# Optimization experiments

Hardware: AMD Instinct MI355X
Metric: run time of the kernel (lower is better)

Reference implementation:

```python
import jax, jax.numpy as jnp
import numpy as np

B, S, D, H, F = 4, 1024, 2048, 16, 8192
HD = D // H  # head dim = 128
EPS = 1e-5


def layer_norm(x, w, b):
    mu = jnp.mean(x, axis=-1, keepdims=True)
    var = jnp.mean(jnp.square(x - mu), axis=-1, keepdims=True)
    return (x - mu) * jax.lax.rsqrt(var + EPS) * w + b


def setup_inputs() -> dict:
    key = jax.random.key(0)
    ks = jax.random.split(key, 12)
    s = 0.02  # realistic init scale for weights
    return {
        "x": jax.random.normal(ks[0], (B, S, D), jnp.float32),
        "attention_mask": jnp.zeros((B, 1, 1, S), jnp.float32),
        "wq": jax.random.normal(ks[1], (D, D), jnp.float32) * s,
        "bq": jax.random.normal(ks[2], (D,), jnp.float32) * s,
        "wk": jax.random.normal(ks[3], (D, D), jnp.float32) * s,
        "bk": jax.random.normal(ks[4], (D,), jnp.float32) * s,
        "wv": jax.random.normal(ks[5], (D, D), jnp.float32) * s,
        "bv": jax.random.normal(ks[6], (D,), jnp.float32) * s,
        "wo": jax.random.normal(ks[7], (D, D), jnp.float32) * s,
        "bo": jax.random.normal(ks[8], (D,), jnp.float32) * s,
        "ln1_w": jnp.ones((D,), jnp.float32),
        "ln1_b": jnp.zeros((D,), jnp.float32),
        "wi": jax.random.normal(ks[9], (F, D), jnp.float32) * s,
        "bi": jax.random.normal(ks[10], (F,), jnp.float32) * s,
        "wo2": jax.random.normal(ks[11], (D, F), jnp.float32) * s,
        "bo2": jnp.zeros((D,), jnp.float32),
        "ln2_w": jnp.ones((D,), jnp.float32),
        "ln2_b": jnp.zeros((D,), jnp.float32),
    }


def reference(x, attention_mask, wq, bq, wk, bk, wv, bv, wo, bo,
              ln1_w, ln1_b, wi, bi, wo2, bo2, ln2_w, ln2_b):
    # --- self attention ---
    q = (jnp.einsum('bsd,ed->bse', x, wq) + bq).reshape(B, S, H, HD).transpose(0, 2, 1, 3)
    k = (jnp.einsum('bsd,ed->bse', x, wk) + bk).reshape(B, S, H, HD).transpose(0, 2, 1, 3)
    v = (jnp.einsum('bsd,ed->bse', x, wv) + bv).reshape(B, S, H, HD).transpose(0, 2, 1, 3)
    scores = jnp.einsum('bhqd,bhkd->bhqk', q, k) / jnp.sqrt(jnp.float32(HD))
    scores = scores + attention_mask  # additive mask, broadcast over heads/query
    probs = jax.nn.softmax(scores, axis=-1)
    ctx = jnp.einsum('bhqk,bhkd->bhqd', probs, v)
    ctx = ctx.transpose(0, 2, 1, 3).reshape(B, S, D)
    # --- attention output: dense + bias + residual + LayerNorm ---
    attn_out = layer_norm(jnp.einsum('bsd,ed->bse', ctx, wo) + bo + x, ln1_w, ln1_b)
    # --- FFN: intermediate dense + bias, GELU, output dense + bias + residual + LN ---
    inter = jnp.einsum('bsd,fd->bsf', attn_out, wi) + bi
    h = jax.nn.gelu(inter, approximate=False)
    out = layer_norm(jnp.einsum('bsf,df->bsd', h, wo2) + bo2 + attn_out, ln2_w, ln2_b)
    return out
```

## Files before the change

kernel.cpp:

```cpp
#include <hip/hip_runtime.h>
#include <hip/hip_bf16.h>
#include <cstdint>
#include <cstddef>

typedef __attribute__((ext_vector_type(8))) short short8;
typedef __attribute__((ext_vector_type(4))) float f32x4;

#define DEV static __device__ __forceinline__

constexpr int kS = 1024, kD = 2048, kH = 16, kHD = 128, kF = 8192;
constexpr int kM = 4096;
constexpr float kEPS = 1e-5f;

constexpr size_t SZ_DD   = (size_t)kD * kD * 2;
constexpr size_t SZ_FD   = (size_t)kF * kD * 2;
constexpr size_t SZ_MD16 = (size_t)kM * kD * 2;
constexpr size_t SZ_MD32 = (size_t)kM * kD * 4;
constexpr size_t OFF_WQ  = 0;
constexpr size_t OFF_WK  = OFF_WQ + SZ_DD;
constexpr size_t OFF_WV  = OFF_WK + SZ_DD;
constexpr size_t OFF_WO  = OFF_WV + SZ_DD;
constexpr size_t OFF_WI  = OFF_WO + SZ_DD;
constexpr size_t OFF_WO2 = OFF_WI + SZ_FD;
constexpr size_t OFF_XB  = OFF_WO2 + SZ_FD;
constexpr size_t OFF_Q   = OFF_XB + SZ_MD16;
constexpr size_t OFF_K   = OFF_Q + SZ_MD16;
constexpr size_t OFF_V   = OFF_K + SZ_MD16;
constexpr size_t OFF_H   = OFF_XB;
constexpr size_t OFF_CTX = OFF_V + SZ_MD16;
constexpr size_t OFF_Y1  = OFF_CTX + SZ_MD16;
constexpr size_t OFF_A1B = OFF_Y1 + SZ_MD32;
constexpr size_t OFF_Y2  = OFF_A1B + SZ_MD16;
constexpr size_t WS_NEED = OFF_Y2 + SZ_MD32;

DEV void gload16(const void* g, void* l) {
  __builtin_amdgcn_global_load_lds(
      (const __attribute__((address_space(1))) unsigned int*)g,
      (__attribute__((address_space(3))) unsigned int*)l, 16, 0, 0);
}

__global__ void cvt_bf16(const float* __restrict__ in, __hip_bfloat16* __restrict__ out, int n4) {
  int stride = gridDim.x * blockDim.x;
  for (int i = blockIdx.x * blockDim.x + threadIdx.x; i < n4; i += stride) {
    float4 v = reinterpret_cast<const float4*>(in)[i];
    union { ushort4 u; __hip_bfloat16 h[4]; } o;
    o.h[0] = __float2bfloat16(v.x);
    o.h[1] = __float2bfloat16(v.y);
    o.h[2] = __float2bfloat16(v.z);
    o.h[3] = __float2bfloat16(v.w);
    reinterpret_cast<ushort4*>(out)[i] = o.u;
  }
}

template <int MODE>
__global__ __launch_bounds__(512, 2)
void gemm256(const __hip_bfloat16* __restrict__ A,
             const __hip_bfloat16* __restrict__ Bt,
             const float* __restrict__ bias,
             float* __restrict__ out0, float* __restrict__ out1,
             void* __restrict__ outb,
             int M, int N, int K, int kLen) {
  __shared__ __align__(16) char lds[131072];
  const int tid = threadIdx.x;
  const int lane = tid & 63, w = tid >> 6;
  const int wm = w >> 2, wn = w & 3;
  const int hw = w >> 2;
  const int lg = lane >> 4, lr = lane & 15;
  const int gy = M >> 8, gx = N >> 8;
  const int nwg = gridDim.x, orig = blockIdx.x;
  const int l = (orig & 7) * (nwg >> 3) + (orig >> 3);
  const int tilesPer = gx * gy;
  const int spl = l / tilesPer;
  const int rem = l - spl * tilesPer;
  const int bx = rem / gy, by = rem - bx * gy;
  const int m0 = by * 256, n0 = bx * 256;
  const int k0 = spl * kLen;
  const int NT = kLen >> 6;

  const char* gs[8];
  #pragma unroll
  for (int h = 0; h < 4; ++h) {
    const __hip_bfloat16* src = (h < 2) ? A : Bt;
    const int r0 = ((h < 2) ? m0 : n0) + (h & 1) * 128;
    #pragma unroll
    for (int i = 0; i < 2; ++i) {
      int c = i * 512 + tid;
      int row = c >> 3, slot = c & 7;
      gs[h * 2 + i] =
          (const char*)(src + (size_t)(r0 + row) * K + k0 + (slot ^ (row & 7)) * 8);
    }
  }

#define STAGE(P, H, TOFF)                                                          \
  {                                                                                \
    char* dstb = lds + (((H) < 2) ? 0 : 65536) + (P) * 32768 + ((H) & 1) * 16384;  \
    gload16(gs[(H) * 2 + 0] + (TOFF) * 128, dstb + (0 * 512 + tid) * 16);          \
    gload16(gs[(H) * 2 + 1] + (TOFF) * 128, dstb + (1 * 512 + tid) * 16);          \
  }

  auto ldA = [&](int P, int qm, int mr, int kk) {
    int row = qm * 128 + wm * 64 + mr * 16 + lr;
    return *reinterpret_cast<const short8*>(
        lds + P * 32768 + row * 128 + (((kk * 4 + lg) ^ (row & 7)) * 16));
  };
  auto ldB = [&](int P, int qn, int nr, int kk) {
    int row = qn * 128 + wn * 32 + nr * 16 + lr;
    return *reinterpret_cast<const short8*>(
        lds + 65536 + P * 32768 + row * 128 + (((kk * 4 + lg) ^ (row & 7)) * 16));
  };

  f32x4 acc[4][4][2] = {};

#define MFMA_HALF(p, kk, B)                                                     \
  _Pragma("unroll")                                                             \
  for (int mi = 0; mi < 4; ++mi)                                                \
    _Pragma("unroll")                                                           \
    for (int ni = 0; ni < 2; ++ni)                                              \
      acc[p][mi][ni] = __builtin_amdgcn_mfma_f32_16x16x32_bf16(                 \
          av[kk][mi], B[kk][ni], acc[p][mi][ni], 0, 0, 0);

#define WAIT_LGKM(n)                                                            \
  asm volatile("s_waitcnt lgkmcnt(" #n ")" ::: "memory");                       \
  __builtin_amdgcn_sched_barrier(0);

#define TILE_BODY(P, PF)                                                        \
  {                                                                             \
          \
    asm volatile("s_waitcnt vmcnt(0)" ::: "memory");                            \
    __builtin_amdgcn_s_barrier();                                               \
                          \
    _Pragma("unroll")                                                           \
    for (int i = 0; i < 4; ++i) av[0][i] = ldA(P, hw, i, 0);                    \
    _Pragma("unroll")                                                           \
    for (int i = 0; i < 2; ++i) b0[0][i] = ldB(P, hw, i, 0);                    \
    _Pragma("unroll")                                                           \
    for (int i = 0; i < 4; ++i) av[1][i] = ldA(P, hw, i, 1);                    \
    _Pragma("unroll")                                                           \
    for (int i = 0; i < 2; ++i) b0[1][i] = ldB(P, hw, i, 1);                    \
    if (PF) { STAGE((P) ^ 1, 0, 1 + (P)) STAGE((P) ^ 1, 2, 1 + (P)) }           \
    WAIT_LGKM(6)                                                                \
    __builtin_amdgcn_s_setprio(1);                                              \
    MFMA_HALF(0, 0, b0)                                                         \
    WAIT_LGKM(0)                                                                \
    MFMA_HALF(0, 1, b0)                                                         \
    __builtin_amdgcn_s_setprio(0);                                              \
                        \
    _Pragma("unroll")                                                           \
    for (int i = 0; i < 2; ++i) b1[0][i] = ldB(P, 1 - hw, i, 0);                \
    _Pragma("unroll")                                                           \
    for (int i = 0; i < 2; ++i) b1[1][i] = ldB(P, 1 - hw, i, 1);                \
    if (PF) { STAGE((P) ^ 1, 3, 1 + (P)) STAGE((P) ^ 1, 1, 1 + (P)) }           \
    WAIT_LGKM(2)                                                                \
    __builtin_amdgcn_s_setprio(1);                                              \
    MFMA_HALF(1, 0, b1)                                                         \
    WAIT_LGKM(0)                                                                \
    MFMA_HALF(1, 1, b1)                                                         \
    __builtin_amdgcn_s_setprio(0);                                              \
                                           \
    _Pragma("unroll")                                                           \
    for (int i = 0; i < 4; ++i) av[0][i] = ldA(P, 1 - hw, i, 0);                \
    _Pragma("unroll")                                                           \
    for (int i = 0; i < 4; ++i) av[1][i] = ldA(P, 1 - hw, i, 1);                \
    WAIT_LGKM(4)                                                                \
    __builtin_amdgcn_s_setprio(1);                                              \
    MFMA_HALF(2, 0, b1)                                                         \
    WAIT_LGKM(0)                                                                \
    MFMA_HALF(2, 1, b1)                                                         \
    __builtin_amdgcn_s_setprio(0);                                              \
                                          \
    _Pragma("unroll")                                                           \
    for (int i = 0; i < 2; ++i) b0[0][i] = ldB(P, hw, i, 0);                    \
    _Pragma("unroll")                                                           \
    for (int i = 0; i < 2; ++i) b0[1][i] = ldB(P, hw, i, 1);                    \
    WAIT_LGKM(2)                                                                \
    __builtin_amdgcn_s_setprio(1);                                              \
    MFMA_HALF(3, 0, b0)                                                         \
    WAIT_LGKM(0)                                                                \
    MFMA_HALF(3, 1, b0)                                                         \
    __builtin_amdgcn_s_setprio(0);                                              \
  }

  STAGE(0, 0, 0) STAGE(0, 2, 0) STAGE(0, 3, 0) STAGE(0, 1, 0)

  for (int t2 = 0; t2 < NT; t2 += 2) {
    short8 av[2][4], b0[2][2], b1[2][2];
    TILE_BODY(0, true)
    TILE_BODY(1, (t2 + 2 < NT))
    #pragma unroll
    for (int j = 0; j < 8; ++j) gs[j] += 256;
  }
#undef TILE_BODY
#undef MFMA_HALF
#undef WAIT_LGKM
#undef STAGE

  #pragma unroll
  for (int p = 0; p < 4; ++p) {
    const int qm = (p < 2) ? hw : 1 - hw;
    const int qn = (p == 0 || p == 3) ? hw : 1 - hw;
    #pragma unroll
    for (int ni = 0; ni < 2; ++ni) {
      int col = n0 + qn * 128 + wn * 32 + ni * 16 + lr;
      float bvv = 0.f;
      if constexpr (MODE != 3) bvv = bias[col];
      #pragma unroll
      for (int mi = 0; mi < 4; ++mi) {
        int row0 = m0 + qm * 128 + wm * 64 + mi * 16 + lg * 4;
        #pragma unroll
        for (int r = 0; r < 4; ++r) {
          int row = row0 + r;
          float val = acc[p][mi][ni][r] + bvv;
          if constexpr (MODE == 0) {
            int which = col >> 11;
            int d = col & 2047;
            int hh = d >> 7, hd = d & 127;
            int bb = row >> 10, ss = row & 1023;
            __hip_bfloat16* base = (__hip_bfloat16*)outb + (size_t)which * ((size_t)kM * kD);
            base[(((size_t)(bb * kH + hh)) * kS + ss) * kHD + hd] = __float2bfloat16(val);
          } else if constexpr (MODE == 2) {
            float g = 0.5f * val * (1.0f + erff(val * 0.70710678118654752f));
            ((__hip_bfloat16*)outb)[(size_t)row * N + col] = __float2bfloat16(g);
          } else {
            float* o = spl ? out1 : out0;
            o[(size_t)row * N + col] = val;
          }
        }
      }
    }
  }
}

__global__ __launch_bounds__(512, 4)
void attn_fwd(const __hip_bfloat16* __restrict__ q,
              const __hip_bfloat16* __restrict__ k,
              const __hip_bfloat16* __restrict__ v,
              const float* __restrict__ mask,
              __hip_bfloat16* __restrict__ ctx) {
  __shared__ __align__(16) char Ks[2][64 * 256];
  __shared__ __align__(16) char Vt[2][128 * 128];
  __shared__ __align__(16) char Ps[8][2048];
  const int tid = threadIdx.x, lane = tid & 63, w = tid >> 6;
  const int lg = lane >> 4, lr = lane & 15;
  const int orig = blockIdx.x;
  const int l = (orig & 7) * 64 + (orig >> 3);
  const int qt = l & 7, bh = l >> 3;
  const int b = bh >> 4;
  const int s4 = tid >> 5, hd4 = tid & 31;

  short8 qf[4];
  {
    const __hip_bfloat16* qp =
        q + ((size_t)bh * kS + qt * 128 + w * 16 + lr) * kHD + lg * 8;
    #pragma unroll
    for (int kk = 0; kk < 4; ++kk) qf[kk] = *reinterpret_cast<const short8*>(qp + kk * 32);
  }

  auto stageK = [&](int bufi, int t) {
    #pragma unroll
    for (int i = 0; i < 2; ++i) {
      int c = i * 512 + tid;
      int row = c >> 4, slot = c & 15;
      gload16(k + ((size_t)bh * kS + t * 64 + row) * kHD + (slot ^ (row & 15)) * 8,
              Ks[bufi] + c * 16);
    }
  };
  union VU { uint2 u; ushort s[4]; };
  VU vr[4];
  auto loadV = [&](int t) {
    #pragma unroll
    for (int i = 0; i < 4; ++i)
      vr[i].u = *reinterpret_cast<const uint2*>(
          v + ((size_t)bh * kS + t * 64 + s4 * 4 + i) * kHD + hd4 * 4);
  };
  auto writeV = [&](int bufi) {
    #pragma unroll
    for (int j = 0; j < 4; ++j) {
      int hd = hd4 * 4 + j;
      ushort4 o;
      o.x = vr[0].s[j]; o.y = vr[1].s[j]; o.z = vr[2].s[j]; o.w = vr[3].s[j];
      *reinterpret_cast<ushort4*>(
          Vt[bufi] + hd * 128 + (((s4 >> 1) ^ (hd & 7)) << 4) + ((s4 & 1) << 3)) = o;
    }
  };

  f32x4 o[8] = {};
  float mrun[4], lrun[4];
  #pragma unroll
  for (int r = 0; r < 4; ++r) { mrun[r] = -1e30f; lrun[r] = 0.f; }
  const float scale = 0.08838834764831845f;

  stageK(0, 0);
  loadV(0);
  writeV(0);
  __syncthreads();

  int buf = 0;
  for (int t = 0; t < 16; ++t) {
    if (t + 1 < 16) { stageK(buf ^ 1, t + 1); loadV(t + 1); }

    f32x4 sacc[4] = {};
    #pragma unroll
    for (int j = 0; j < 4; ++j) {
      int key = j * 16 + lr;
      #pragma unroll
      for (int kk = 0; kk < 4; ++kk) {
        short8 bfrag = *reinterpret_cast<const short8*>(
            Ks[buf] + key * 256 + (((kk * 4 + lg) ^ (key & 15)) * 16));
        sacc[j] = __builtin_amdgcn_mfma_f32_16x16x32_bf16(qf[kk], bfrag, sacc[j], 0, 0, 0);
      }
    }
    float sarr[4][4];
    #pragma unroll
    for (int j = 0; j < 4; ++j) {
      float mv = mask[(size_t)b * kS + t * 64 + j * 16 + lr];
      #pragma unroll
      for (int r = 0; r < 4; ++r) sarr[j][r] = sacc[j][r] * scale + mv;
    }
    #pragma unroll
    for (int r = 0; r < 4; ++r) {
      float tm = fmaxf(fmaxf(sarr[0][r], sarr[1][r]), fmaxf(sarr[2][r], sarr[3][r]));
      #pragma unroll
      for (int d = 1; d < 16; d <<= 1) tm = fmaxf(tm, __shfl_xor(tm, d));
      float mnew = fmaxf(mrun[r], tm);
      float alpha = __expf(mrun[r] - mnew);
      mrun[r] = mnew;
      float rs = 0.f;
      #pragma unroll
      for (int j = 0; j < 4; ++j) {
        float p = __expf(sarr[j][r] - mnew);
        sarr[j][r] = p;
        rs += p;
      }
      #pragma unroll
      for (int d = 1; d < 16; d <<= 1) rs += __shfl_xor(rs, d);
      lrun[r] = lrun[r] * alpha + rs;
      #pragma unroll
      for (int n = 0; n < 8; ++n) o[n][r] *= alpha;
    }
    #pragma unroll
    for (int r = 0; r < 4; ++r) {
      int qr = lg * 4 + r;
      #pragma unroll
      for (int j = 0; j < 4; ++j)
        *reinterpret_cast<__hip_bfloat16*>(
            Ps[w] + ((qr * 128 + (j * 16 + lr) * 2) ^ ((qr & 7) << 4))) =
            __float2bfloat16(sarr[j][r]);
    }
    #pragma unroll
    for (int kk2 = 0; kk2 < 2; ++kk2) {
      short8 pa = *reinterpret_cast<const short8*>(
          Ps[w] + ((lr * 128 + kk2 * 64 + lg * 16) ^ ((lr & 7) << 4)));
      #pragma unroll
      for (int n = 0; n < 8; ++n) {
        int hd = n * 16 + lr;
        short8 vb = *reinterpret_cast<const short8*>(
            Vt[buf] + hd * 128 + (((kk2 * 4 + lg) ^ (hd & 7)) * 16));
        o[n] = __builtin_amdgcn_mfma_f32_16x16x32_bf16(pa, vb, o[n], 0, 0, 0);
      }
    }
    if (t + 1 < 16) writeV(buf ^ 1);
    __syncthreads();
    buf ^= 1;
  }

  const int h = bh & 15;
  #pragma unroll
  for (int r = 0; r < 4; ++r) {
    float inv = 1.0f / lrun[r];
    int srow = qt * 128 + w * 16 + lg * 4 + r;
    __hip_bfloat16* cp = ctx + ((size_t)b * kS + srow) * kD + h * 128 + lr;
    #pragma unroll
    for (int n = 0; n < 8; ++n) cp[n * 16] = __float2bfloat16(o[n][r] * inv);
  }
}

template <bool WB16>
__global__ void ln_fuse(const float* __restrict__ p0, const float* __restrict__ p1,
                        const float* __restrict__ bias, const float* __restrict__ res,
                        const float* __restrict__ w, const float* __restrict__ b,
                        float* __restrict__ outf, __hip_bfloat16* __restrict__ outb) {
  const int row = blockIdx.x, tid = threadIdx.x;
  const size_t base = (size_t)row * kD;
  float v[8];
  #pragma unroll
  for (int i = 0; i < 2; ++i) {
    int c4 = tid * 2 + i;
    float4 a  = reinterpret_cast<const float4*>(p0 + base)[c4];
    float4 bb = reinterpret_cast<const float4*>(p1 + base)[c4];
    float4 rr = reinterpret_cast<const float4*>(res + base)[c4];
    float4 bs = reinterpret_cast<const float4*>(bias)[c4];
    v[i * 4 + 0] = a.x + bb.x + rr.x + bs.x;
    v[i * 4 + 1] = a.y + bb.y + rr.y + bs.y;
    v[i * 4 + 2] = a.z + bb.z + rr.z + bs.z;
    v[i * 4 + 3] = a.w + bb.w + rr.w + bs.w;
  }
  float s = 0.f;
  #pragma unroll
  for (int i = 0; i < 8; ++i) s += v[i];
  #pragma unroll
  for (int off = 32; off > 0; off >>= 1) s += __shfl_down(s, off);
  __shared__ float r1[4], r2[4];
  if ((tid & 63) == 0) r1[tid >> 6] = s;
  __syncthreads();
  float mean = (r1[0] + r1[1] + r1[2] + r1[3]) * (1.0f / kD);
  float qv = 0.f;
  #pragma unroll
  for (int i = 0; i < 8; ++i) { float d = v[i] - mean; qv += d * d; }
  #pragma unroll
  for (int off = 32; off > 0; off >>= 1) qv += __shfl_down(qv, off);
  if ((tid & 63) == 0) r2[tid >> 6] = qv;
  __syncthreads();
  float rstd = rsqrtf((r2[0] + r2[1] + r2[2] + r2[3]) * (1.0f / kD) + kEPS);
  #pragma unroll
  for (int i = 0; i < 8; ++i) {
    int col = tid * 8 + i;
    float ov = (v[i] - mean) * rstd * w[col] + b[col];
    outf[base + col] = ov;
    if constexpr (WB16) outb[base + col] = __float2bfloat16(ov);
  }
}

extern "C" void kernel_launch(void* const* d_in, const int* in_sizes, int n_in,
                              void* d_out, int out_size, void* d_ws, size_t ws_size,
                              hipStream_t stream) {
  (void)in_sizes; (void)n_in; (void)out_size;
  if (ws_size < WS_NEED) return;
  const float* x    = (const float*)d_in[0];
  const float* mask = (const float*)d_in[1];
  const float* wq   = (const float*)d_in[2];
  const float* bq   = (const float*)d_in[3];
  const float* wk   = (const float*)d_in[4];
  const float* bk   = (const float*)d_in[5];
  const float* wv   = (const float*)d_in[6];
  const float* bv   = (const float*)d_in[7];
  const float* wo   = (const float*)d_in[8];
  const float* bo   = (const float*)d_in[9];
  const float* l1w  = (const float*)d_in[10];
  const float* l1b  = (const float*)d_in[11];
  const float* wi   = (const float*)d_in[12];
  const float* bi   = (const float*)d_in[13];
  const float* wo2  = (const float*)d_in[14];
  const float* bo2  = (const float*)d_in[15];
  const float* l2w  = (const float*)d_in[16];
  const float* l2b  = (const float*)d_in[17];

  char* ws = (char*)d_ws;
  __hip_bfloat16* wqb  = (__hip_bfloat16*)(ws + OFF_WQ);
  __hip_bfloat16* wkb  = (__hip_bfloat16*)(ws + OFF_WK);
  __hip_bfloat16* wvb  = (__hip_bfloat16*)(ws + OFF_WV);
  __hip_bfloat16* wob  = (__hip_bfloat16*)(ws + OFF_WO);
  __hip_bfloat16* wib  = (__hip_bfloat16*)(ws + OFF_WI);
  __hip_bfloat16* wo2b = (__hip_bfloat16*)(ws + OFF_WO2);
  __hip_bfloat16* xb   = (__hip_bfloat16*)(ws + OFF_XB);
  __hip_bfloat16* qb   = (__hip_bfloat16*)(ws + OFF_Q);
  __hip_bfloat16* kb2  = (__hip_bfloat16*)(ws + OFF_K);
  __hip_bfloat16* vb2  = (__hip_bfloat16*)(ws + OFF_V);
  __hip_bfloat16* hb   = (__hip_bfloat16*)(ws + OFF_H);
  __hip_bfloat16* ctxb = (__hip_bfloat16*)(ws + OFF_CTX);
  __hip_bfloat16* a1b  = (__hip_bfloat16*)(ws + OFF_A1B);
  float* y1   = (float*)(ws + OFF_Y1);
  float* y2   = (float*)(ws + OFF_Y2);
  float* f2p  = (float*)(ws + OFF_WQ);
  float* bqkv = (float*)(ws + OFF_Y2);

  cvt_bf16<<<2048, 256, 0, stream>>>(x,   xb,   kM * kD / 4);
  cvt_bf16<<<1024, 256, 0, stream>>>(wq,  wqb,  kD * kD / 4);
  cvt_bf16<<<1024, 256, 0, stream>>>(wk,  wkb,  kD * kD / 4);
  cvt_bf16<<<1024, 256, 0, stream>>>(wv,  wvb,  kD * kD / 4);
  cvt_bf16<<<1024, 256, 0, stream>>>(wo,  wob,  kD * kD / 4);
  cvt_bf16<<<2048, 256, 0, stream>>>(wi,  wib,  kF * kD / 4);
  cvt_bf16<<<2048, 256, 0, stream>>>(wo2, wo2b, kF * kD / 4);
  hipMemcpyAsync(bqkv,          bq, kD * 4, hipMemcpyDeviceToDevice, stream);
  hipMemcpyAsync(bqkv + kD,     bk, kD * 4, hipMemcpyDeviceToDevice, stream);
  hipMemcpyAsync(bqkv + 2 * kD, bv, kD * 4, hipMemcpyDeviceToDevice, stream);

  dim3 blk(512);
  gemm256<0><<<dim3(384), blk, 0, stream>>>(
      xb, wqb, bqkv, nullptr, nullptr, qb, kM, 6144, kD, kD);
  attn_fwd<<<dim3(512), dim3(512), 0, stream>>>(qb, kb2, vb2, mask, ctxb);
  gemm256<3><<<dim3(256), blk, 0, stream>>>(
      ctxb, wob, nullptr, y1, y2, nullptr, kM, kD, kD, kD / 2);
  ln_fuse<true><<<kM, 256, 0, stream>>>(y1, y2, bo, x, l1w, l1b, y1, a1b);
  gemm256<2><<<dim3(512), blk, 0, stream>>>(
      a1b, wib, bi, nullptr, nullptr, hb, kM, kF, kD, kD);
  gemm256<3><<<dim3(256), blk, 0, stream>>>(
      hb, wo2b, nullptr, y2, f2p, nullptr, kM, kD, kF, kF / 2);
  ln_fuse<false><<<kM, 256, 0, stream>>>(y2, f2p, bo2, y1, l2w, l2b, (float*)d_out, nullptr);
}
```

Baseline: 672.5 us.

## Merge conversion kernels into one launch and double query rows per attention block

Replaces seven fp32-to-bf16 conversion launches plus three bias memcpys with a single cvt_all kernel that walks the contiguous workspace layout. The attention kernel now processes two 128-row query sub-tiles per block (256 blocks instead of 512), reusing each staged K/V tile for twice as many queries to halve K/V load and transpose work. The cost is doubled accumulator and softmax state per thread, which lowers occupancy (launch bounds drop from 4 to 2 blocks) and leaves fewer blocks to spread across CUs.

Measured after the change: 604.6 us. -10.1%, faster.

```diff
diff --git a/kernel.cpp b/kernel.cpp
--- a/kernel.cpp
+++ b/kernel.cpp
@@ -39,16 +39,37 @@
       (__attribute__((address_space(3))) unsigned int*)l, 16, 0, 0);
 }
 
-__global__ void cvt_bf16(const float* __restrict__ in, __hip_bfloat16* __restrict__ out, int n4) {
+__global__ void cvt_all(const float* __restrict__ x,  const float* __restrict__ wq,
+                        const float* __restrict__ wk, const float* __restrict__ wv,
+                        const float* __restrict__ wo, const float* __restrict__ wi,
+                        const float* __restrict__ wo2,
+                        const float* __restrict__ bq, const float* __restrict__ bk,
+                        const float* __restrict__ bv,
+                        __hip_bfloat16* __restrict__ outw, float* __restrict__ bqkv) {
+  constexpr int M1 = 1 << 20;
+  constexpr int NW = 14 * M1;
   int stride = gridDim.x * blockDim.x;
-  for (int i = blockIdx.x * blockDim.x + threadIdx.x; i < n4; i += stride) {
-    float4 v = reinterpret_cast<const float4*>(in)[i];
-    union { ushort4 u; __hip_bfloat16 h[4]; } o;
-    o.h[0] = __float2bfloat16(v.x);
-    o.h[1] = __float2bfloat16(v.y);
-    o.h[2] = __float2bfloat16(v.z);
-    o.h[3] = __float2bfloat16(v.w);
-    reinterpret_cast<ushort4*>(out)[i] = o.u;
+  for (int i = blockIdx.x * blockDim.x + threadIdx.x; i < NW + 1536; i += stride) {
+    if (i < NW) {
+      const float* src; int off;
+      if (i < 4 * M1)       { src = (i < M1) ? wq : (i < 2 * M1) ? wk : (i < 3 * M1) ? wv : wo;
+                              off = i & (M1 - 1); }
+      else if (i < 8 * M1)  { src = wi;  off = i - 4 * M1; }
+      else if (i < 12 * M1) { src = wo2; off = i - 8 * M1; }
+      else                  { src = x;   off = i - 12 * M1; }
+      float4 v = reinterpret_cast<const float4*>(src)[off];
+      union { ushort4 u; __hip_bfloat16 h[4]; } o;
+      o.h[0] = __float2bfloat16(v.x);
+      o.h[1] = __float2bfloat16(v.y);
+      o.h[2] = __float2bfloat16(v.z);
+      o.h[3] = __float2bfloat16(v.w);
+      reinterpret_cast<ushort4*>(outw)[i] = o.u;
+    } else {
+      int j = i - NW;
+      const float* src = (j < 512) ? bq : (j < 1024) ? bk : bv;
+      reinterpret_cast<float4*>(bqkv)[j] =
+          reinterpret_cast<const float4*>(src)[j & 511];
+    }
   }
 }
 
@@ -125,10 +146,8 @@
 
 #define TILE_BODY(P, PF)                                                        \
   {                                                                             \
-          \
     asm volatile("s_waitcnt vmcnt(0)" ::: "memory");                            \
     __builtin_amdgcn_s_barrier();                                               \
-                          \
     _Pragma("unroll")                                                           \
     for (int i = 0; i < 4; ++i) av[0][i] = ldA(P, hw, i, 0);                    \
     _Pragma("unroll")                                                           \
@@ -144,7 +163,6 @@
     WAIT_LGKM(0)                                                                \
     MFMA_HALF(0, 1, b0)                                                         \
     __builtin_amdgcn_s_setprio(0);                                              \
-                        \
     _Pragma("unroll")                                                           \
     for (int i = 0; i < 2; ++i) b1[0][i] = ldB(P, 1 - hw, i, 0);                \
     _Pragma("unroll")                                                           \
@@ -156,7 +174,6 @@
     WAIT_LGKM(0)                                                                \
     MFMA_HALF(1, 1, b1)                                                         \
     __builtin_amdgcn_s_setprio(0);                                              \
-                                           \
     _Pragma("unroll")                                                           \
     for (int i = 0; i < 4; ++i) av[0][i] = ldA(P, 1 - hw, i, 0);                \
     _Pragma("unroll")                                                           \
@@ -167,7 +184,6 @@
     WAIT_LGKM(0)                                                                \
     MFMA_HALF(2, 1, b1)                                                         \
     __builtin_amdgcn_s_setprio(0);                                              \
-                                          \
     _Pragma("unroll")                                                           \
     for (int i = 0; i < 2; ++i) b0[0][i] = ldB(P, hw, i, 0);                    \
     _Pragma("unroll")                                                           \
@@ -230,7 +246,7 @@
   }
 }
 
-__global__ __launch_bounds__(512, 4)
+__global__ __launch_bounds__(512, 2)
 void attn_fwd(const __hip_bfloat16* __restrict__ q,
               const __hip_bfloat16* __restrict__ k,
               const __hip_bfloat16* __restrict__ v,
@@ -242,17 +258,19 @@
   const int tid = threadIdx.x, lane = tid & 63, w = tid >> 6;
   const int lg = lane >> 4, lr = lane & 15;
   const int orig = blockIdx.x;
-  const int l = (orig & 7) * 64 + (orig >> 3);
-  const int qt = l & 7, bh = l >> 3;
+  const int l = (orig & 7) * 32 + (orig >> 3);
+  const int qp = l & 3, bh = l >> 2;
   const int b = bh >> 4;
   const int s4 = tid >> 5, hd4 = tid & 31;
 
-  short8 qf[4];
-  {
-    const __hip_bfloat16* qp =
-        q + ((size_t)bh * kS + qt * 128 + w * 16 + lr) * kHD + lg * 8;
-    #pragma unroll
-    for (int kk = 0; kk < 4; ++kk) qf[kk] = *reinterpret_cast<const short8*>(qp + kk * 32);
+  short8 qf[2][4];
+  #pragma unroll
+  for (int s = 0; s < 2; ++s) {
+    const __hip_bfloat16* qp_ =
+        q + ((size_t)bh * kS + qp * 256 + s * 128 + w * 16 + lr) * kHD + lg * 8;
+    #pragma unroll
+    for (int kk = 0; kk < 4; ++kk)
+      qf[s][kk] = *reinterpret_cast<const short8*>(qp_ + kk * 32);
   }
 
   auto stageK = [&](int bufi, int t) {
@@ -276,17 +294,19 @@
     #pragma unroll
     for (int j = 0; j < 4; ++j) {
       int hd = hd4 * 4 + j;
-      ushort4 o;
-      o.x = vr[0].s[j]; o.y = vr[1].s[j]; o.z = vr[2].s[j]; o.w = vr[3].s[j];
+      ushort4 o4;
+      o4.x = vr[0].s[j]; o4.y = vr[1].s[j]; o4.z = vr[2].s[j]; o4.w = vr[3].s[j];
       *reinterpret_cast<ushort4*>(
-          Vt[bufi] + hd * 128 + (((s4 >> 1) ^ (hd & 7)) << 4) + ((s4 & 1) << 3)) = o;
+          Vt[bufi] + hd * 128 + (((s4 >> 1) ^ (hd & 7)) << 4) + ((s4 & 1) << 3)) = o4;
     }
   };
 
-  f32x4 o[8] = {};
-  float mrun[4], lrun[4];
-  #pragma unroll
-  for (int r = 0; r < 4; ++r) { mrun[r] = -1e30f; lrun[r] = 0.f; }
+  f32x4 o[2][8] = {};
+  float mrun[2][4], lrun[2][4];
+  #pragma unroll
+  for (int s = 0; s < 2; ++s)
+    #pragma unroll
+    for (int r = 0; r < 4; ++r) { mrun[s][r] = -1e30f; lrun[s][r] = 0.f; }
   const float scale = 0.08838834764831845f;
 
   stageK(0, 0);
@@ -298,64 +318,69 @@
   for (int t = 0; t < 16; ++t) {
     if (t + 1 < 16) { stageK(buf ^ 1, t + 1); loadV(t + 1); }
 
-    f32x4 sacc[4] = {};
-    #pragma unroll
-    for (int j = 0; j < 4; ++j) {
-      int key = j * 16 + lr;
-      #pragma unroll
-      for (int kk = 0; kk < 4; ++kk) {
-        short8 bfrag = *reinterpret_cast<const short8*>(
-            Ks[buf] + key * 256 + (((kk * 4 + lg) ^ (key & 15)) * 16));
-        sacc[j] = __builtin_amdgcn_mfma_f32_16x16x32_bf16(qf[kk], bfrag, sacc[j], 0, 0, 0);
+    float mv[4];
+    #pragma unroll
+    for (int j = 0; j < 4; ++j) mv[j] = mask[(size_t)b * kS + t * 64 + j * 16 + lr];
+
+    #pragma unroll
+    for (int s = 0; s < 2; ++s) {
+      f32x4 sacc[4] = {};
+      #pragma unroll
+      for (int j = 0; j < 4; ++j) {
+        int key = j * 16 + lr;
+        #pragma unroll
+        for (int kk = 0; kk < 4; ++kk) {
+          short8 bfrag = *reinterpret_cast<const short8*>(
+              Ks[buf] + key * 256 + (((kk * 4 + lg) ^ (key & 15)) * 16));
+          sacc[j] = __builtin_amdgcn_mfma_f32_16x16x32_bf16(qf[s][kk], bfrag, sacc[j], 0, 0, 0);
+        }
       }
-    }
-    float sarr[4][4];
-    #pragma unroll
-    for (int j = 0; j < 4; ++j) {
-      float mv = mask[(size_t)b * kS + t * 64 + j * 16 + lr];
-      #pragma unroll
-      for (int r = 0; r < 4; ++r) sarr[j][r] = sacc[j][r] * scale + mv;
-    }
-    #pragma unroll
-    for (int r = 0; r < 4; ++r) {
-      float tm = fmaxf(fmaxf(sarr[0][r], sarr[1][r]), fmaxf(sarr[2][r], sarr[3][r]));
-      #pragma unroll
-      for (int d = 1; d < 16; d <<= 1) tm = fmaxf(tm, __shfl_xor(tm, d));
-      float mnew = fmaxf(mrun[r], tm);
-      float alpha = __expf(mrun[r] - mnew);
-      mrun[r] = mnew;
-      float rs = 0.f;
-      #pragma unroll
-      for (int j = 0; j < 4; ++j) {
-        float p = __expf(sarr[j][r] - mnew);
-        sarr[j][r] = p;
-        rs += p;
+      float sarr[4][4];
+      #pragma unroll
+      for (int j = 0; j < 4; ++j)
+        #pragma unroll
+        for (int r = 0; r < 4; ++r) sarr[j][r] = sacc[j][r] * scale + mv[j];
+      #pragma unroll
+      for (int r = 0; r < 4; ++r) {
+        float tm = fmaxf(fmaxf(sarr[0][r], sarr[1][r]), fmaxf(sarr[2][r], sarr[3][r]));
+        #pragma unroll
+        for (int d = 1; d < 16; d <<= 1) tm = fmaxf(tm, __shfl_xor(tm, d));
+        float mnew = fmaxf(mrun[s][r], tm);
+        float alpha = __expf(mrun[s][r] - mnew);
+        mrun[s][r] = mnew;
+        float rs = 0.f;
+        #pragma unroll
+        for (int j = 0; j < 4; ++j) {
+          float p = __expf(sarr[j][r] - mnew);
+          sarr[j][r] = p;
+          rs += p;
+        }
+        #pragma unroll
+        for (int d = 1; d < 16; d <<= 1) rs += __shfl_xor(rs, d);
+        lrun[s][r] = lrun[s][r] * alpha + rs;
+        #pragma unroll
+        for (int n = 0; n < 8; ++n) o[s][n][r] *= alpha;
       }
       #pragma unroll
-      for (int d = 1; d < 16; d <<= 1) rs += __shfl_xor(rs, d);
-      lrun[r] = lrun[r] * alpha + rs;
-      #pragma unroll
-      for (int n = 0; n < 8; ++n) o[n][r] *= alpha;
-    }
-    #pragma unroll
-    for (int r = 0; r < 4; ++r) {
-      int qr = lg * 4 + r;
-      #pragma unroll
-      for (int j = 0; j < 4; ++j)
-        *reinterpret_cast<__hip_bfloat16*>(
-            Ps[w] + ((qr * 128 + (j * 16 + lr) * 2) ^ ((qr & 7) << 4))) =
-            __float2bfloat16(sarr[j][r]);
-    }
-    #pragma unroll
-    for (int kk2 = 0; kk2 < 2; ++kk2) {
-      short8 pa = *reinterpret_cast<const short8*>(
-          Ps[w] + ((lr * 128 + kk2 * 64 + lg * 16) ^ ((lr & 7) << 4)));
-      #pragma unroll
-      for (int n = 0; n < 8; ++n) {
-        int hd = n * 16 + lr;
-        short8 vb = *reinterpret_cast<const short8*>(
-            Vt[buf] + hd * 128 + (((kk2 * 4 + lg) ^ (hd & 7)) * 16));
-        o[n] = __builtin_amdgcn_mfma_f32_16x16x32_bf16(pa, vb, o[n], 0, 0, 0);
+      for (int r = 0; r < 4; ++r) {
+        int qr = lg * 4 + r;
+        #pragma unroll
+        for (int j = 0; j < 4; ++j)
+          *reinterpret_cast<__hip_bfloat16*>(
+              Ps[w] + ((qr * 128 + (j * 16 + lr) * 2) ^ ((qr & 7) << 4))) =
+              __float2bfloat16(sarr[j][r]);
+      }
+      #pragma unroll
+      for (int kk2 = 0; kk2 < 2; ++kk2) {
+        short8 pa = *reinterpret_cast<const short8*>(
+            Ps[w] + ((lr * 128 + kk2 * 64 + lg * 16) ^ ((lr & 7) << 4)));
+        #pragma unroll
+        for (int n = 0; n < 8; ++n) {
+          int hd = n * 16 + lr;
+          short8 vb = *reinterpret_cast<const short8*>(
+              Vt[buf] + hd * 128 + (((kk2 * 4 + lg) ^ (hd & 7)) * 16));
+          o[s][n] = __builtin_amdgcn_mfma_f32_16x16x32_bf16(pa, vb, o[s][n], 0, 0, 0);
+        }
       }
     }
     if (t + 1 < 16) writeV(buf ^ 1);
@@ -365,13 +390,15 @@
 
   const int h = bh & 15;
   #pragma unroll
-  for (int r = 0; r < 4; ++r) {
-    float inv = 1.0f / lrun[r];
-    int srow = qt * 128 + w * 16 + lg * 4 + r;
-    __hip_bfloat16* cp = ctx + ((size_t)b * kS + srow) * kD + h * 128 + lr;
-    #pragma unroll
-    for (int n = 0; n < 8; ++n) cp[n * 16] = __float2bfloat16(o[n][r] * inv);
-  }
+  for (int s = 0; s < 2; ++s)
+    #pragma unroll
+    for (int r = 0; r < 4; ++r) {
+      float inv = 1.0f / lrun[s][r];
+      int srow = qp * 256 + s * 128 + w * 16 + lg * 4 + r;
+      __hip_bfloat16* cp = ctx + ((size_t)b * kS + srow) * kD + h * 128 + lr;
+      #pragma unroll
+      for (int n = 0; n < 8; ++n) cp[n * 16] = __float2bfloat16(o[s][n][r] * inv);
+    }
 }
 
 template <bool WB16>
@@ -446,8 +473,6 @@
 
   char* ws = (char*)d_ws;
   __hip_bfloat16* wqb  = (__hip_bfloat16*)(ws + OFF_WQ);
-  __hip_bfloat16* wkb  = (__hip_bfloat16*)(ws + OFF_WK);
-  __hip_bfloat16* wvb  = (__hip_bfloat16*)(ws + OFF_WV);
   __hip_bfloat16* wob  = (__hip_bfloat16*)(ws + OFF_WO);
   __hip_bfloat16* wib  = (__hip_bfloat16*)(ws + OFF_WI);
   __hip_bfloat16* wo2b = (__hip_bfloat16*)(ws + OFF_WO2);
@@ -463,21 +488,12 @@
   float* f2p  = (float*)(ws + OFF_WQ);
   float* bqkv = (float*)(ws + OFF_Y2);
 
-  cvt_bf16<<<2048, 256, 0, stream>>>(x,   xb,   kM * kD / 4);
-  cvt_bf16<<<1024, 256, 0, stream>>>(wq,  wqb,  kD * kD / 4);
-  cvt_bf16<<<1024, 256, 0, stream>>>(wk,  wkb,  kD * kD / 4);
-  cvt_bf16<<<1024, 256, 0, stream>>>(wv,  wvb,  kD * kD / 4);
-  cvt_bf16<<<1024, 256, 0, stream>>>(wo,  wob,  kD * kD / 4);
-  cvt_bf16<<<2048, 256, 0, stream>>>(wi,  wib,  kF * kD / 4);
-  cvt_bf16<<<2048, 256, 0, stream>>>(wo2, wo2b, kF * kD / 4);
-  hipMemcpyAsync(bqkv,          bq, kD * 4, hipMemcpyDeviceToDevice, stream);
-  hipMemcpyAsync(bqkv + kD,     bk, kD * 4, hipMemcpyDeviceToDevice, stream);
-  hipMemcpyAsync(bqkv + 2 * kD, bv, kD * 4, hipMemcpyDeviceToDevice, stream);
+  cvt_all<<<2048, 256, 0, stream>>>(x, wq, wk, wv, wo, wi, wo2, bq, bk, bv, wqb, bqkv);
 
   dim3 blk(512);
   gemm256<0><<<dim3(384), blk, 0, stream>>>(
       xb, wqb, bqkv, nullptr, nullptr, qb, kM, 6144, kD, kD);
-  attn_fwd<<<dim3(512), dim3(512), 0, stream>>>(qb, kb2, vb2, mask, ctxb);
+  attn_fwd<<<dim3(256), dim3(512), 0, stream>>>(qb, kb2, vb2, mask, ctxb);
   gemm256<3><<<dim3(256), blk, 0, stream>>>(
       ctxb, wob, nullptr, y1, y2, nullptr, kM, kD, kD, kD / 2);
   ln_fuse<true><<<kM, 256, 0, stream>>>(y1, y2, bo, x, l1w, l1b, y1, a1b);
```
